# Optimization experiments

Measured on AMD Instinct MI355X. Metric: run time of the kernel, lower is better.

## Reference

```python
import jax, jax.numpy as jnp
import numpy as np

B, N = 4096, 29
NC, CD, HD, L = 6, 16, 64, 2   # num_classes, context_dim, hidden_dim(m_dim), gnn layers
D = NC + CD                    # 22, node feature dim
IDX0, IDX1 = 0, 2
OUT = (IDX1 - IDX0) * NC * 2   # 24
EPS = 1e-5


def setup_inputs() -> dict:
    key = jax.random.key(0)
    ks = jax.random.split(key, 20)
    g = lambda k, shape, fan_in: jax.random.normal(k, shape, jnp.float32) / np.sqrt(fan_in)
    return {
        "x": jax.random.normal(ks[0], (B, N, NC), jnp.float32),
        "context": jax.random.normal(ks[1], (B, N, CD), jnp.float32),
        # per-layer GNN params, stacked on leading layer axis
        "eW1": g(ks[2], (L, 2 * D, HD), 2 * D), "eb1": jnp.zeros((L, HD)),
        "eW2": g(ks[3], (L, HD, HD), HD),       "eb2": jnp.zeros((L, HD)),
        "gW":  g(ks[4], (L, HD, 1), HD),        "gb":  jnp.zeros((L, 1)),
        "ln_g": jnp.ones((L, D)),               "ln_b": jnp.zeros((L, D)),
        "nW1": g(ks[5], (L, D + HD, HD), D + HD), "nb1": jnp.zeros((L, HD)),
        "nW2": g(ks[6], (L, HD, D), HD),        "nb2": jnp.zeros((L, D)),
        # head MLP
        "hW1": g(ks[7], (D, HD), D), "hb1": jnp.zeros((HD,)),
        "hW2": g(ks[8], (HD, OUT), HD), "hb2": jnp.zeros((OUT,)),
    }


def _layernorm(z, gamma, beta):
    mu = jnp.mean(z, axis=-1, keepdims=True)
    var = jnp.var(z, axis=-1, keepdims=True)
    return (z - mu) * jax.lax.rsqrt(var + EPS) * gamma + beta


def _gnn_layer(z, eW1, eb1, eW2, eb2, gW, gb, ln_g, ln_b, nW1, nb1, nW2, nb2):
    # edge_mlp on concat(z_i, z_j): split the first weight to avoid materializing [B,N,N,2D]
    pi = jnp.einsum('bnd,dm->bnm', z, eW1[:D])       # source-half projection
    pj = jnp.einsum('bnd,dm->bnm', z, eW1[D:])       # target-half projection
    m = jax.nn.silu(pi[:, :, None, :] + pj[:, None, :, :] + eb1)   # [B,N,N,HD]
    m = jax.nn.silu(jnp.einsum('bijm,mk->bijk', m, eW2) + eb2)
    gate = jax.nn.sigmoid(jnp.einsum('bijm,mo->bijo', m, gW) + gb)  # soft edges
    m_i = jnp.sum(m * gate, axis=2)                  # aggregate over neighbors j -> [B,N,HD]
    zn = _layernorm(z, ln_g, ln_b)                   # norm_feats=True
    h = jax.nn.silu(jnp.einsum('bnd,dm->bnm', jnp.concatenate([zn, m_i], -1), nW1) + nb1)
    h = jnp.einsum('bnm,md->bnd', h, nW2) + nb2
    return z + h                                      # residual


def reference(x, context, eW1, eb1, eW2, eb2, gW, gb, ln_g, ln_b,
              nW1, nb1, nW2, nb2, hW1, hb1, hW2, hb2):
    z = jnp.concatenate([x, context], axis=-1)        # [B,N,D]
    for l in range(L):
        z = _gnn_layer(z, eW1[l], eb1[l], eW2[l], eb2[l], gW[l], gb[l],
                       ln_g[l], ln_b[l], nW1[l], nb1[l], nW2[l], nb2[l])
    z = jnp.mean(z, axis=1)                           # mean pool over nodes -> [B,D]
    z = jax.nn.relu(z @ hW1 + hb1)
    z = (z @ hW2 + hb2).reshape(B, IDX1 - IDX0, NC * 2)
    z = jnp.pad(z, ((0, 0), (IDX0, 29 - IDX1), (0, 0)))  # pad node axis to 29
    return z
```

## Files before the change

kernel.cpp:

```cpp
#include <hip/hip_runtime.h>
#include <hip/hip_bf16.h>

typedef __attribute__((ext_vector_type(8))) short short8;
typedef __attribute__((ext_vector_type(4))) float f32x4;

__device__ __forceinline__ float fsigmoid(float x) {
  return __builtin_amdgcn_rcpf(1.0f + __expf(-x));
}
__device__ __forceinline__ float fsilu(float x) { return x * fsigmoid(x); }
__device__ __forceinline__ unsigned short bf16b(float x) {
  union { float f; unsigned u; } c; c.f = x;
  unsigned r = c.u + 0x7FFFu + ((c.u >> 16) & 1u);
  return (unsigned short)(r >> 16);
}
__device__ __forceinline__ float b2f(unsigned short u) {
  union { unsigned v; float f; } c; c.v = ((unsigned)u) << 16; return c.f;
}
__device__ __forceinline__ short8 pack8(const float* v) {
  short8 r;
  #pragma unroll
  for (int m = 0; m < 4; ++m) {
    __hip_bfloat162 h = __float22bfloat162_rn(make_float2(v[2 * m], v[2 * m + 1]));
    short2 s2 = *reinterpret_cast<const short2*>(&h);
    r[2 * m] = s2.x; r[2 * m + 1] = s2.y;
  }
  return r;
}
template<int CTRL>
__device__ __forceinline__ float dpp_add(float x) {
  int xi = __builtin_bit_cast(int, x);
  int yi = __builtin_amdgcn_update_dpp(0, xi, CTRL, 0xF, 0xF, true);
  return x + __builtin_bit_cast(float, yi);
}
__device__ __forceinline__ float row16_sum(float x) {
  x = dpp_add<0x121>(x);
  x = dpp_add<0x122>(x);
  x = dpp_add<0x124>(x);
  x = dpp_add<0x128>(x);
  return x;
}

__global__ void setup_kernel(const float* __restrict__ eW1, const float* __restrict__ eW2,
                             const float* __restrict__ nW1, const float* __restrict__ nW2,
                             unsigned short* __restrict__ WS) {
  int t = blockIdx.x * 256 + threadIdx.x;
  float val = 0.f;
  if (t < 8192) {
    int l = t >> 12, r = t & 4095;
    int nt = r >> 9, lane = (r >> 3) & 63, e = r & 7;
    int k = 8 * (lane >> 4) + e, n = 16 * nt + (lane & 15);
    if (k < 22) val = (n < 64) ? eW1[l * 2816 + k * 64 + n]
                               : eW1[l * 2816 + (22 + k) * 64 + (n - 64)];
  } else if (t < 16384) {
    int u = t - 8192;
    int l = u >> 12, r = u & 4095;
    int ks = r >> 11, nt = (r >> 9) & 3, lane = (r >> 3) & 63, e = r & 7;
    int k = 32 * ks + 8 * (lane >> 4) + e, n = 16 * nt + (lane & 15);
    val = eW2[l * 4096 + k * 64 + n];
  } else if (t < 28672) {
    int u = t - 16384;
    int l = u / 6144, r = u % 6144;
    int ks = r >> 11, nt = (r >> 9) & 3, lane = (r >> 3) & 63, e = r & 7;
    int k = 32 * ks + 8 * (lane >> 4) + e, n = 16 * nt + (lane & 15);
    if (k < 86) val = nW1[l * 5504 + k * 64 + n];
  } else {
    int u = t - 28672;
    int l = u >> 11, r = u & 2047;
    int ks = r >> 10, nt = (r >> 9) & 1, lane = (r >> 3) & 63, e = r & 7;
    int k = 32 * ks + 8 * (lane >> 4) + e, n = 16 * nt + (lane & 15);
    if (n < 22) val = nW2[l * 1408 + k * 22 + n];
  }
  WS[t] = bf16b(val);
}

__launch_bounds__(256, 4)
__global__ void proj_kernel(const float* __restrict__ X, const float* __restrict__ CTX,
                            const unsigned short* __restrict__ WS,
                            const float* __restrict__ EB1,
                            const float* __restrict__ LNG, const float* __restrict__ LNB,
                            float* __restrict__ Z, unsigned short* __restrict__ SPP,
                            unsigned short* __restrict__ CIN, int l)
{
  __shared__ float sz[29 * 36];
  const int b = blockIdx.x, tid = threadIdx.x;
  const int lane = tid & 63, w = tid >> 6;
  const int lr = lane & 15, lg = lane >> 4, kb = lg * 8;

  if (l == 0) {
    for (int t = tid; t < 29 * 36; t += 256) {
      int i = t / 36, c = t - i * 36;
      float v = 0.f;
      if (c < 6) v = X[b * 174 + i * 6 + c];
      else if (c < 22) v = CTX[b * 464 + i * 16 + (c - 6)];
      sz[t] = v;
      if (c < 32) Z[(b * 29 + i) * 32 + c] = v;
    }
  } else {
    for (int t = tid; t < 29 * 36; t += 256) {
      int i = t / 36, c = t - i * 36;
      sz[t] = (c < 32) ? Z[(b * 29 + i) * 32 + c] : 0.f;
    }
  }
  __syncthreads();

  {
    int rt = w >> 1;
    int rowc = min(16 * rt + lr, 28);
    float zr[8];
    *(float4*)&zr[0] = *(const float4*)&sz[rowc * 36 + kb];
    *(float4*)&zr[4] = *(const float4*)&sz[rowc * 36 + kb + 4];
    short8 af = pack8(zr);
    int ntb = 4 * (w & 1);
    const unsigned short* wp = WS + (l * 4096 + ntb * 512 + lane * 8);
    #pragma unroll
    for (int t = 0; t < 4; ++t) {
      short8 bfr = *(const short8*)(wp + t * 512);
      f32x4 zz = {0.f, 0.f, 0.f, 0.f};
      f32x4 acc = __builtin_amdgcn_mfma_f32_16x16x32_bf16(af, bfr, zz, 0, 0, 0);
      int n = 16 * (ntb + t) + lr;
      float bias = (ntb + t < 4) ? EB1[l * 64 + n] : 0.f;
      #pragma unroll
      for (int r = 0; r < 4; ++r) {
        int orow = 16 * rt + 4 * lg + r;
        if (orow < 29) SPP[(b * 29 + orow) * 128 + n] = bf16b(acc[r] + bias);
      }
    }
  }
  if (w == 3 && lane < 29) {
    const float* row = &sz[lane * 36];
    float s = 0.f, q = 0.f;
    #pragma unroll
    for (int c4 = 0; c4 < 6; ++c4) {
      float4 v = *(const float4*)(row + 4 * c4);
      s += v.x + v.y + v.z + v.w;
      q += v.x * v.x + v.y * v.y + v.z * v.z + v.w * v.w;
    }
    float mu = s * (1.f / 22.f);
    float var = q * (1.f / 22.f) - mu * mu;
    float rr = rsqrtf(var + 1e-5f);
    unsigned short* crow = CIN + (b * 29 + lane) * 96;
    #pragma unroll
    for (int d = 0; d < 22; ++d)
      crow[d] = bf16b((row[d] - mu) * rr * LNG[l * 22 + d] + LNB[l * 22 + d]);
    #pragma unroll
    for (int d = 86; d < 96; ++d) crow[d] = 0;
  }
}

__launch_bounds__(256, 2)
__global__ void edge_kernel(const unsigned short* __restrict__ WS,
                            const unsigned short* __restrict__ SPP,
                            const float* __restrict__ EB2, const float* __restrict__ GW,
                            const float* __restrict__ GB,
                            unsigned short* __restrict__ CIN, int l)
{
  const int tid = threadIdx.x;
  const int lane = tid & 63, w = tid >> 6;
  const int lr = lane & 15, lg = lane >> 4, kb = lg * 8;
  const int wid = blockIdx.x * 4 + w;
  const int b = (int)((unsigned)wid / 29u);
  const int i = wid - b * 29;

  const unsigned short* wp = WS + (8192 + l * 4096 + lane * 8);
  short8 w2f[2][4];
  #pragma unroll
  for (int s = 0; s < 2; ++s)
    #pragma unroll
    for (int t = 0; t < 4; ++t)
      w2f[s][t] = *(const short8*)(wp + s * 2048 + t * 512);
  float eb2c[4], gwc[4];
  #pragma unroll
  for (int t = 0; t < 4; ++t) {
    eb2c[t] = EB2[l * 64 + 16 * t + lr];
    gwc[t]  = GW [l * 64 + 16 * t + lr];
  }
  const float gbv = GB[l];

  const unsigned short* pirow = SPP + (b * 29 + i) * 128 + kb;
  short8 pib0 = *(const short8*)(pirow);
  short8 pib1 = *(const short8*)(pirow + 32);
  float pif[2][8];
  #pragma unroll
  for (int m = 0; m < 8; ++m) { pif[0][m] = b2f(pib0[m]); pif[1][m] = b2f(pib1[m]); }

  float macc[4] = {0.f, 0.f, 0.f, 0.f};

  #pragma unroll
  for (int tb = 0; tb < 2; ++tb) {
    const int jb = tb * 16;
    const int ja = min(jb + lr, 28);
    const unsigned short* pjrow = SPP + (b * 29 + ja) * 128 + 64 + kb;
    short8 pjb0 = *(const short8*)(pjrow);
    short8 pjb1 = *(const short8*)(pjrow + 32);
    float m1[8];
    #pragma unroll
    for (int m = 0; m < 8; ++m) m1[m] = fsilu(pif[0][m] + b2f(pjb0[m]));
    short8 af0 = pack8(m1);
    #pragma unroll
    for (int m = 0; m < 8; ++m) m1[m] = fsilu(pif[1][m] + b2f(pjb1[m]));
    short8 af1 = pack8(m1);

    f32x4 a0 = {0.f,0.f,0.f,0.f}, a1 = {0.f,0.f,0.f,0.f};
    f32x4 a2 = {0.f,0.f,0.f,0.f}, a3 = {0.f,0.f,0.f,0.f};
    a0 = __builtin_amdgcn_mfma_f32_16x16x32_bf16(af0, w2f[0][0], a0, 0, 0, 0);
    a1 = __builtin_amdgcn_mfma_f32_16x16x32_bf16(af0, w2f[0][1], a1, 0, 0, 0);
    a2 = __builtin_amdgcn_mfma_f32_16x16x32_bf16(af0, w2f[0][2], a2, 0, 0, 0);
    a3 = __builtin_amdgcn_mfma_f32_16x16x32_bf16(af0, w2f[0][3], a3, 0, 0, 0);
    a0 = __builtin_amdgcn_mfma_f32_16x16x32_bf16(af1, w2f[1][0], a0, 0, 0, 0);
    a1 = __builtin_amdgcn_mfma_f32_16x16x32_bf16(af1, w2f[1][1], a1, 0, 0, 0);
    a2 = __builtin_amdgcn_mfma_f32_16x16x32_bf16(af1, w2f[1][2], a2, 0, 0, 0);
    a3 = __builtin_amdgcn_mfma_f32_16x16x32_bf16(af1, w2f[1][3], a3, 0, 0, 0);

    float m2v[4][4];
    #pragma unroll
    for (int r = 0; r < 4; ++r) {
      m2v[0][r] = fsilu(a0[r] + eb2c[0]);
      m2v[1][r] = fsilu(a1[r] + eb2c[1]);
      m2v[2][r] = fsilu(a2[r] + eb2c[2]);
      m2v[3][r] = fsilu(a3[r] + eb2c[3]);
    }
    float g0 = m2v[0][0]*gwc[0] + m2v[1][0]*gwc[1] + m2v[2][0]*gwc[2] + m2v[3][0]*gwc[3];
    float g1 = m2v[0][1]*gwc[0] + m2v[1][1]*gwc[1] + m2v[2][1]*gwc[2] + m2v[3][1]*gwc[3];
    float g2 = m2v[0][2]*gwc[0] + m2v[1][2]*gwc[1] + m2v[2][2]*gwc[2] + m2v[3][2]*gwc[3];
    float g3 = m2v[0][3]*gwc[0] + m2v[1][3]*gwc[1] + m2v[2][3]*gwc[2] + m2v[3][3]*gwc[3];
    g0 = row16_sum(g0); g1 = row16_sum(g1); g2 = row16_sum(g2); g3 = row16_sum(g3);
    float gg[4] = {g0, g1, g2, g3};
    #pragma unroll
    for (int r = 0; r < 4; ++r) {
      int jrow = jb + 4 * lg + r;
      float gv = (jrow < 29) ? fsigmoid(gg[r] + gbv) : 0.f;
      macc[0] += m2v[0][r] * gv;
      macc[1] += m2v[1][r] * gv;
      macc[2] += m2v[2][r] * gv;
      macc[3] += m2v[3][r] * gv;
    }
  }

  float red0 = macc[0], red1 = macc[1], red2 = macc[2], red3 = macc[3];
  red0 += __shfl_xor(red0, 16, 64); red0 += __shfl_xor(red0, 32, 64);
  red1 += __shfl_xor(red1, 16, 64); red1 += __shfl_xor(red1, 32, 64);
  red2 += __shfl_xor(red2, 16, 64); red2 += __shfl_xor(red2, 32, 64);
  red3 += __shfl_xor(red3, 16, 64); red3 += __shfl_xor(red3, 32, 64);
  float vs = (lg == 0) ? red0 : (lg == 1) ? red1 : (lg == 2) ? red2 : red3;
  CIN[(b * 29 + i) * 96 + 22 + lane] = bf16b(vs);
}

__launch_bounds__(256, 4)
__global__ void node_kernel(const unsigned short* __restrict__ WS,
                            const unsigned short* __restrict__ CIN,
                            const float* __restrict__ NB1, const float* __restrict__ NB2,
                            float* __restrict__ Z,
                            const float* __restrict__ HW1, const float* __restrict__ HB1,
                            const float* __restrict__ HW2, const float* __restrict__ HB2,
                            float* __restrict__ OUTP, int l)
{
  __shared__ float sz[29 * 32];
  __shared__ float sh1[29 * 68];
  __shared__ float szm[22], shh[64], sob[24];
  const int b = blockIdx.x, tid = threadIdx.x;
  const int lane = tid & 63, w = tid >> 6;
  const int lr = lane & 15, lg = lane >> 4, kb = lg * 8;

  for (int t = tid; t < 29 * 8; t += 256)
    ((float4*)sz)[t] = ((const float4*)(Z + b * 29 * 32))[t];
  __syncthreads();

  {
    int rt = w >> 1;
    int ntb = 2 * (w & 1);
    int rowc = min(16 * rt + lr, 28);
    const unsigned short* arow = CIN + (b * 29 + rowc) * 96 + kb;
    const unsigned short* wp = WS + (16384 + l * 6144 + ntb * 512 + lane * 8);
    f32x4 acc[2] = {{0.f,0.f,0.f,0.f}, {0.f,0.f,0.f,0.f}};
    #pragma unroll
    for (int s = 0; s < 3; ++s) {
      short8 af = *(const short8*)(arow + 32 * s);
      #pragma unroll
      for (int t = 0; t < 2; ++t) {
        short8 bfr = *(const short8*)(wp + s * 2048 + t * 512);
        acc[t] = __builtin_amdgcn_mfma_f32_16x16x32_bf16(af, bfr, acc[t], 0, 0, 0);
      }
    }
    #pragma unroll
    for (int t = 0; t < 2; ++t) {
      int n = 16 * (ntb + t) + lr;
      float bias = NB1[l * 64 + n];
      #pragma unroll
      for (int r = 0; r < 4; ++r) {
        int orow = 16 * rt + 4 * lg + r;
        if (orow < 29) sh1[orow * 68 + n] = fsilu(acc[t][r] + bias);
      }
    }
  }
  __syncthreads();

  {
    int rt = w & 1;
    int nt = w >> 1;
    int rowc = min(16 * rt + lr, 28);
    int d = 16 * nt + lr;
    const unsigned short* wp = WS + (28672 + l * 2048 + nt * 512 + lane * 8);
    f32x4 acc = {0.f, 0.f, 0.f, 0.f};
    #pragma unroll
    for (int s = 0; s < 2; ++s) {
      float ar[8];
      *(float4*)&ar[0] = *(const float4*)&sh1[rowc * 68 + kb + 32 * s];
      *(float4*)&ar[4] = *(const float4*)&sh1[rowc * 68 + kb + 32 * s + 4];
      short8 af = pack8(ar);
      short8 bfr = *(const short8*)(wp + s * 1024);
      acc = __builtin_amdgcn_mfma_f32_16x16x32_bf16(af, bfr, acc, 0, 0, 0);
    }
    float bias = (d < 22) ? NB2[l * 22 + d] : 0.f;
    #pragma unroll
    for (int r = 0; r < 4; ++r) {
      int orow = 16 * rt + 4 * lg + r;
      if (orow < 29 && d < 22) sz[orow * 32 + d] += acc[r] + bias;
    }
  }
  __syncthreads();

  if (l == 0) {
    for (int t = tid; t < 29 * 8; t += 256)
      ((float4*)(Z + b * 29 * 32))[t] = ((const float4*)sz)[t];
  } else {
    if (tid < 22) {
      float s = 0.f;
      #pragma unroll
      for (int i = 0; i < 29; ++i) s += sz[i * 32 + tid];
      szm[tid] = s * (1.f / 29.f);
    }
    __syncthreads();
    if (tid < 64) {
      float a = HB1[tid];
      #pragma unroll
      for (int d = 0; d < 22; ++d) a += szm[d] * HW1[d * 64 + tid];
      shh[tid] = fmaxf(a, 0.f);
    }
    __syncthreads();
    if (tid < 24) {
      float a = HB2[tid];
      #pragma unroll
      for (int m = 0; m < 64; ++m) a += shh[m] * HW2[m * 24 + tid];
      sob[tid] = a;
    }
    __syncthreads();
    for (int t = tid; t < 29 * 12; t += 256)
      OUTP[b * 348 + t] = (t < 24) ? sob[t] : 0.f;
  }
}

extern "C" void kernel_launch(void* const* d_in, const int* in_sizes, int n_in,
                              void* d_out, int out_size, void* d_ws, size_t ws_size,
                              hipStream_t stream) {
  const float* X   = (const float*)d_in[0];
  const float* CTX = (const float*)d_in[1];
  const float* EW1 = (const float*)d_in[2];
  const float* EB1 = (const float*)d_in[3];
  const float* EW2 = (const float*)d_in[4];
  const float* EB2 = (const float*)d_in[5];
  const float* GW  = (const float*)d_in[6];
  const float* GB  = (const float*)d_in[7];
  const float* LNG = (const float*)d_in[8];
  const float* LNB = (const float*)d_in[9];
  const float* NW1 = (const float*)d_in[10];
  const float* NB1 = (const float*)d_in[11];
  const float* NW2 = (const float*)d_in[12];
  const float* NB2 = (const float*)d_in[13];
  const float* HW1 = (const float*)d_in[14];
  const float* HB1 = (const float*)d_in[15];
  const float* HW2 = (const float*)d_in[16];
  const float* HB2 = (const float*)d_in[17];
  float* OUTP = (float*)d_out;

  unsigned short* WS = (unsigned short*)d_ws;
  float* Z = (float*)((char*)d_ws + 65536);
  unsigned short* SPP = (unsigned short*)((char*)d_ws + 65536 + 15204352);
  unsigned short* CIN = (unsigned short*)((char*)d_ws + 65536 + 15204352 + 30408704);

  hipLaunchKernelGGL(setup_kernel, dim3(128), dim3(256), 0, stream,
                     EW1, EW2, NW1, NW2, WS);
  for (int l = 0; l < 2; ++l) {
    hipLaunchKernelGGL(proj_kernel, dim3(4096), dim3(256), 0, stream,
                       X, CTX, WS, EB1, LNG, LNB, Z, SPP, CIN, l);
    hipLaunchKernelGGL(edge_kernel, dim3(4096 * 29 / 4), dim3(256), 0, stream,
                       WS, SPP, EB2, GW, GB, CIN, l);
    hipLaunchKernelGGL(node_kernel, dim3(4096), dim3(256), 0, stream,
                       WS, CIN, NB1, NB2, Z, HW1, HB1, HW2, HB2, OUTP, l);
  }
}
```

Measured before the change: 389.8 us.

## Assign one wave per graph in edge kernel, reusing target projections across nodes

The edge kernel now maps each wavefront to a whole graph instead of to a single (graph, node) pair. The wave loads the target-half projections and the W2 fragments once, then loops over all 29 source nodes. The grid shrinks from 29696 to 1024 blocks. This amortises the weight and projection loads and the per-wave setup, but the loop is serial with unroll 1, and 4096 waves may give too little parallelism to hide latency on the GPU.

```diff
diff --git a/kernel.cpp b/kernel.cpp
--- a/kernel.cpp
+++ b/kernel.cpp
@@ -157,9 +157,7 @@
   const int tid = threadIdx.x;
   const int lane = tid & 63, w = tid >> 6;
   const int lr = lane & 15, lg = lane >> 4, kb = lg * 8;
-  const int wid = blockIdx.x * 4 + w;
-  const int b = (int)((unsigned)wid / 29u);
-  const int i = wid - b * 29;
+  const int b = blockIdx.x * 4 + w;
 
   const unsigned short* wp = WS + (8192 + l * 4096 + lane * 8);
   short8 w2f[2][4];
@@ -176,73 +174,83 @@
   }
   const float gbv = GB[l];
 
-  const unsigned short* pirow = SPP + (b * 29 + i) * 128 + kb;
-  short8 pib0 = *(const short8*)(pirow);
-  short8 pib1 = *(const short8*)(pirow + 32);
-  float pif[2][8];
-  #pragma unroll
-  for (int m = 0; m < 8; ++m) { pif[0][m] = b2f(pib0[m]); pif[1][m] = b2f(pib1[m]); }
-
-  float macc[4] = {0.f, 0.f, 0.f, 0.f};
-
+  float pjf[2][2][8];
   #pragma unroll
   for (int tb = 0; tb < 2; ++tb) {
-    const int jb = tb * 16;
-    const int ja = min(jb + lr, 28);
+    int ja = min(tb * 16 + lr, 28);
     const unsigned short* pjrow = SPP + (b * 29 + ja) * 128 + 64 + kb;
-    short8 pjb0 = *(const short8*)(pjrow);
-    short8 pjb1 = *(const short8*)(pjrow + 32);
-    float m1[8];
-    #pragma unroll
-    for (int m = 0; m < 8; ++m) m1[m] = fsilu(pif[0][m] + b2f(pjb0[m]));
-    short8 af0 = pack8(m1);
-    #pragma unroll
-    for (int m = 0; m < 8; ++m) m1[m] = fsilu(pif[1][m] + b2f(pjb1[m]));
-    short8 af1 = pack8(m1);
-
-    f32x4 a0 = {0.f,0.f,0.f,0.f}, a1 = {0.f,0.f,0.f,0.f};
-    f32x4 a2 = {0.f,0.f,0.f,0.f}, a3 = {0.f,0.f,0.f,0.f};
-    a0 = __builtin_amdgcn_mfma_f32_16x16x32_bf16(af0, w2f[0][0], a0, 0, 0, 0);
-    a1 = __builtin_amdgcn_mfma_f32_16x16x32_bf16(af0, w2f[0][1], a1, 0, 0, 0);
-    a2 = __builtin_amdgcn_mfma_f32_16x16x32_bf16(af0, w2f[0][2], a2, 0, 0, 0);
-    a3 = __builtin_amdgcn_mfma_f32_16x16x32_bf16(af0, w2f[0][3], a3, 0, 0, 0);
-    a0 = __builtin_amdgcn_mfma_f32_16x16x32_bf16(af1, w2f[1][0], a0, 0, 0, 0);
-    a1 = __builtin_amdgcn_mfma_f32_16x16x32_bf16(af1, w2f[1][1], a1, 0, 0, 0);
-    a2 = __builtin_amdgcn_mfma_f32_16x16x32_bf16(af1, w2f[1][2], a2, 0, 0, 0);
-    a3 = __builtin_amdgcn_mfma_f32_16x16x32_bf16(af1, w2f[1][3], a3, 0, 0, 0);
-
-    float m2v[4][4];
-    #pragma unroll
-    for (int r = 0; r < 4; ++r) {
-      m2v[0][r] = fsilu(a0[r] + eb2c[0]);
-      m2v[1][r] = fsilu(a1[r] + eb2c[1]);
-      m2v[2][r] = fsilu(a2[r] + eb2c[2]);
-      m2v[3][r] = fsilu(a3[r] + eb2c[3]);
-    }
-    float g0 = m2v[0][0]*gwc[0] + m2v[1][0]*gwc[1] + m2v[2][0]*gwc[2] + m2v[3][0]*gwc[3];
-    float g1 = m2v[0][1]*gwc[0] + m2v[1][1]*gwc[1] + m2v[2][1]*gwc[2] + m2v[3][1]*gwc[3];
-    float g2 = m2v[0][2]*gwc[0] + m2v[1][2]*gwc[1] + m2v[2][2]*gwc[2] + m2v[3][2]*gwc[3];
-    float g3 = m2v[0][3]*gwc[0] + m2v[1][3]*gwc[1] + m2v[2][3]*gwc[2] + m2v[3][3]*gwc[3];
-    g0 = row16_sum(g0); g1 = row16_sum(g1); g2 = row16_sum(g2); g3 = row16_sum(g3);
-    float gg[4] = {g0, g1, g2, g3};
-    #pragma unroll
-    for (int r = 0; r < 4; ++r) {
-      int jrow = jb + 4 * lg + r;
-      float gv = (jrow < 29) ? fsigmoid(gg[r] + gbv) : 0.f;
-      macc[0] += m2v[0][r] * gv;
-      macc[1] += m2v[1][r] * gv;
-      macc[2] += m2v[2][r] * gv;
-      macc[3] += m2v[3][r] * gv;
-    }
-  }
-
-  float red0 = macc[0], red1 = macc[1], red2 = macc[2], red3 = macc[3];
-  red0 += __shfl_xor(red0, 16, 64); red0 += __shfl_xor(red0, 32, 64);
-  red1 += __shfl_xor(red1, 16, 64); red1 += __shfl_xor(red1, 32, 64);
-  red2 += __shfl_xor(red2, 16, 64); red2 += __shfl_xor(red2, 32, 64);
-  red3 += __shfl_xor(red3, 16, 64); red3 += __shfl_xor(red3, 32, 64);
-  float vs = (lg == 0) ? red0 : (lg == 1) ? red1 : (lg == 2) ? red2 : red3;
-  CIN[(b * 29 + i) * 96 + 22 + lane] = bf16b(vs);
+    short8 p0 = *(const short8*)(pjrow);
+    short8 p1 = *(const short8*)(pjrow + 32);
+    #pragma unroll
+    for (int m = 0; m < 8; ++m) { pjf[tb][0][m] = b2f(p0[m]); pjf[tb][1][m] = b2f(p1[m]); }
+  }
+
+  const unsigned short* pibase = SPP + b * 29 * 128 + kb;
+  unsigned short* cbase = CIN + (b * 29) * 96 + 22 + lane;
+
+  #pragma unroll 1
+  for (int i = 0; i < 29; ++i) {
+    short8 pb0 = *(const short8*)(pibase + i * 128);
+    short8 pb1 = *(const short8*)(pibase + i * 128 + 32);
+    float pif[2][8];
+    #pragma unroll
+    for (int m = 0; m < 8; ++m) { pif[0][m] = b2f(pb0[m]); pif[1][m] = b2f(pb1[m]); }
+
+    float macc[4] = {0.f, 0.f, 0.f, 0.f};
+    #pragma unroll
+    for (int tb = 0; tb < 2; ++tb) {
+      float m1[8];
+      #pragma unroll
+      for (int m = 0; m < 8; ++m) m1[m] = fsilu(pif[0][m] + pjf[tb][0][m]);
+      short8 af0 = pack8(m1);
+      #pragma unroll
+      for (int m = 0; m < 8; ++m) m1[m] = fsilu(pif[1][m] + pjf[tb][1][m]);
+      short8 af1 = pack8(m1);
+
+      f32x4 a0 = {0.f,0.f,0.f,0.f}, a1 = {0.f,0.f,0.f,0.f};
+      f32x4 a2 = {0.f,0.f,0.f,0.f}, a3 = {0.f,0.f,0.f,0.f};
+      a0 = __builtin_amdgcn_mfma_f32_16x16x32_bf16(af0, w2f[0][0], a0, 0, 0, 0);
+      a1 = __builtin_amdgcn_mfma_f32_16x16x32_bf16(af0, w2f[0][1], a1, 0, 0, 0);
+      a2 = __builtin_amdgcn_mfma_f32_16x16x32_bf16(af0, w2f[0][2], a2, 0, 0, 0);
+      a3 = __builtin_amdgcn_mfma_f32_16x16x32_bf16(af0, w2f[0][3], a3, 0, 0, 0);
+      a0 = __builtin_amdgcn_mfma_f32_16x16x32_bf16(af1, w2f[1][0], a0, 0, 0, 0);
+      a1 = __builtin_amdgcn_mfma_f32_16x16x32_bf16(af1, w2f[1][1], a1, 0, 0, 0);
+      a2 = __builtin_amdgcn_mfma_f32_16x16x32_bf16(af1, w2f[1][2], a2, 0, 0, 0);
+      a3 = __builtin_amdgcn_mfma_f32_16x16x32_bf16(af1, w2f[1][3], a3, 0, 0, 0);
+
+      float m2v[4][4];
+      #pragma unroll
+      for (int r = 0; r < 4; ++r) {
+        m2v[0][r] = fsilu(a0[r] + eb2c[0]);
+        m2v[1][r] = fsilu(a1[r] + eb2c[1]);
+        m2v[2][r] = fsilu(a2[r] + eb2c[2]);
+        m2v[3][r] = fsilu(a3[r] + eb2c[3]);
+      }
+      float g0 = m2v[0][0]*gwc[0] + m2v[1][0]*gwc[1] + m2v[2][0]*gwc[2] + m2v[3][0]*gwc[3];
+      float g1 = m2v[0][1]*gwc[0] + m2v[1][1]*gwc[1] + m2v[2][1]*gwc[2] + m2v[3][1]*gwc[3];
+      float g2 = m2v[0][2]*gwc[0] + m2v[1][2]*gwc[1] + m2v[2][2]*gwc[2] + m2v[3][2]*gwc[3];
+      float g3 = m2v[0][3]*gwc[0] + m2v[1][3]*gwc[1] + m2v[2][3]*gwc[2] + m2v[3][3]*gwc[3];
+      g0 = row16_sum(g0); g1 = row16_sum(g1); g2 = row16_sum(g2); g3 = row16_sum(g3);
+      float gg[4] = {g0, g1, g2, g3};
+      #pragma unroll
+      for (int r = 0; r < 4; ++r) {
+        int jrow = tb * 16 + 4 * lg + r;
+        float gv = (jrow < 29) ? fsigmoid(gg[r] + gbv) : 0.f;
+        macc[0] += m2v[0][r] * gv;
+        macc[1] += m2v[1][r] * gv;
+        macc[2] += m2v[2][r] * gv;
+        macc[3] += m2v[3][r] * gv;
+      }
+    }
+
+    float red0 = macc[0], red1 = macc[1], red2 = macc[2], red3 = macc[3];
+    red0 += __shfl_xor(red0, 16, 64); red0 += __shfl_xor(red0, 32, 64);
+    red1 += __shfl_xor(red1, 16, 64); red1 += __shfl_xor(red1, 32, 64);
+    red2 += __shfl_xor(red2, 16, 64); red2 += __shfl_xor(red2, 32, 64);
+    red3 += __shfl_xor(red3, 16, 64); red3 += __shfl_xor(red3, 32, 64);
+    float vs = (lg == 0) ? red0 : (lg == 1) ? red1 : (lg == 2) ? red2 : red3;
+    cbase[i * 96] = bf16b(vs);
+  }
 }
 
 __launch_bounds__(256, 4)
@@ -382,7 +390,7 @@
   for (int l = 0; l < 2; ++l) {
     hipLaunchKernelGGL(proj_kernel, dim3(4096), dim3(256), 0, stream,
                        X, CTX, WS, EB1, LNG, LNB, Z, SPP, CIN, l);
-    hipLaunchKernelGGL(edge_kernel, dim3(4096 * 29 / 4), dim3(256), 0, stream,
+    hipLaunchKernelGGL(edge_kernel, dim3(1024), dim3(256), 0, stream,
                        WS, SPP, EB2, GW, GB, CIN, l);
     hipLaunchKernelGGL(node_kernel, dim3(4096), dim3(256), 0, stream,
                        WS, CIN, NB1, NB2, Z, HW1, HB1, HW2, HB2, OUTP, l);
```

Result: no change. 391.9 us (+0.6%).
